# Optimization experiments

Hardware: AMD Instinct MI355X
Metric: run time of the kernel (lower is better)

The kernel has to match this reference:

```python
import jax, jax.numpy as jnp
import numpy as np

L, B, S, KV, H, D, HID, FF = 4, 16, 16, 2048, 6, 128, 768, 2048


def apply_rope(x, positions, max_wavelength=10000.0):
    # x: [B, S, H, D], positions: [B, S]; computed in float32 as in the torch code
    d_half = x.shape[-1] // 2
    freq_exponents = (2.0 / x.shape[-1]) * jnp.arange(d_half, dtype=jnp.float32)
    timescale = max_wavelength ** freq_exponents  # [d_half]
    radians = positions[..., None].astype(jnp.float32) / timescale[None, None, :]
    radians = radians[..., None, :]  # [B, S, 1, d_half]
    sin, cos = jnp.sin(radians), jnp.cos(radians)
    xf = x.astype(jnp.float32)
    x1, x2 = xf[..., :d_half], xf[..., d_half:]
    out = jnp.concatenate([x1 * cos - x2 * sin, x2 * cos + x1 * sin], axis=-1)
    return out.astype(x.dtype)


def rms_norm(x, w, eps=1e-6):
    var = jnp.mean(jnp.square(x.astype(jnp.float32)), axis=-1, keepdims=True)
    return (x.astype(jnp.float32) * jax.lax.rsqrt(var + eps)).astype(x.dtype) * w


def make_att_2d_masks(pad_masks, att_masks):
    # cumsum-comparison prefix-LM / block-causal mask (big_vision style)
    cumsum = jnp.cumsum(att_masks, axis=1)
    att_2d = cumsum[:, None, :] <= cumsum[:, :, None]
    pad_2d = pad_masks[:, None, :] & pad_masks[:, :, None]
    return att_2d & pad_2d


def setup_inputs() -> dict:
    key = jax.random.key(0)
    ks = jax.random.split(key, 20)
    sc = 0.02
    inputs_embeds = jax.random.normal(ks[0], (B, S, HID), jnp.float32)
    position_ids = jnp.broadcast_to(KV + jnp.arange(S, dtype=jnp.int64)[None, :], (B, S))
    pad_masks = jnp.ones((B, KV + S), dtype=bool)
    # prefix-LM: prefix tokens bidirectional (0), expert suffix causal (1)
    att_masks = jnp.concatenate([jnp.zeros((B, KV), jnp.int32), jnp.ones((B, S), jnp.int32)], axis=1)
    k_cache = jax.random.normal(ks[1], (L, B, H, KV, D), jnp.float32)
    v_cache = jax.random.normal(ks[2], (L, B, H, KV, D), jnp.float32)
    p = {
        'Wq': jax.random.normal(ks[3], (L, HID, H * D), jnp.float32) * sc,
        'bq': jnp.zeros((L, H * D), jnp.float32),
        'Wk': jax.random.normal(ks[4], (L, HID, H * D), jnp.float32) * sc,
        'bk': jnp.zeros((L, H * D), jnp.float32),
        'Wv': jax.random.normal(ks[5], (L, HID, H * D), jnp.float32) * sc,
        'bv': jnp.zeros((L, H * D), jnp.float32),
        'Wo': jax.random.normal(ks[6], (L, H * D, HID), jnp.float32) * sc,
        'Wg': jax.random.normal(ks[7], (L, HID, FF), jnp.float32) * sc,
        'Wu': jax.random.normal(ks[8], (L, HID, FF), jnp.float32) * sc,
        'Wd': jax.random.normal(ks[9], (L, FF, HID), jnp.float32) * sc,
        'ln1': jnp.ones((L, HID), jnp.float32),
        'ln2': jnp.ones((L, HID), jnp.float32),
        'norm_f': jnp.ones((HID,), jnp.float32),
    }
    return dict(inputs_embeds=inputs_embeds, position_ids=position_ids, pad_masks=pad_masks,
                att_masks=att_masks, k_cache=k_cache, v_cache=v_cache, **p)


def reference(inputs_embeds, position_ids, pad_masks, att_masks, k_cache, v_cache,
              Wq, bq, Wk, bk, Wv, bv, Wo, Wg, Wu, Wd, ln1, ln2, norm_f):
    b, s, _ = inputs_embeds.shape
    kv = k_cache.shape[3]
    scale = 1.0 / np.sqrt(D)
    # 2D prefix-lm mask over full prefix+suffix; expert queries are the last s rows
    mask2d = make_att_2d_masks(pad_masks, att_masks)[:, kv:, :]  # [B, S, KV+S]
    bias = jnp.where(mask2d[:, None, :, :], 0.0, -1e9).astype(inputs_embeds.dtype)
    h = inputs_embeds
    for l in range(Wq.shape[0]):
        hn = rms_norm(h, ln1[l])
        q = (hn @ Wq[l] + bq[l]).reshape(b, s, H, D)
        k = (hn @ Wk[l] + bk[l]).reshape(b, s, H, D)
        v = (hn @ Wv[l] + bv[l]).reshape(b, s, H, D)
        q = apply_rope(q, position_ids)
        k = apply_rope(k, position_ids)
        qh = jnp.swapaxes(q, 1, 2)  # [B, H, S, D]
        kf = jnp.concatenate([k_cache[l], jnp.swapaxes(k, 1, 2)], axis=2)  # [B, H, KV+S, D]
        vf = jnp.concatenate([v_cache[l], jnp.swapaxes(v, 1, 2)], axis=2)
        scores = jnp.einsum('bhqd,bhkd->bhqk', qh, kf) * scale + bias
        attn = jax.nn.softmax(scores, axis=-1)
        o = jnp.einsum('bhqk,bhkd->bhqd', attn, vf)
        o = jnp.swapaxes(o, 1, 2).reshape(b, s, H * D) @ Wo[l]
        h = h + o
        hn2 = rms_norm(h, ln2[l])
        h = h + (jax.nn.silu(hn2 @ Wg[l]) * (hn2 @ Wu[l])) @ Wd[l]
    return rms_norm(h, norm_f)
```

## Files before the change

### kernel.cpp

```cpp
#include <hip/hip_runtime.h>
#include <hip/hip_bf16.h>

#define LNUM 4
#define BB 16
#define SS 16
#define KVC 2048
#define HH 6
#define DD 128
#define HIDN 768
#define FFN 2048
#define NCH 17
#define ATT_SCALE 0.08838834764831845f
#define VT_PAD 136
#define OSH_PAD 132
#define AP 776
#define AP3 1032

typedef unsigned short u16;
typedef short s16x8 __attribute__((ext_vector_type(8)));
typedef unsigned short u16x4 __attribute__((ext_vector_type(4)));
typedef float f32x4 __attribute__((ext_vector_type(4)));

__device__ __forceinline__ short f2bfs(float f) {
    __hip_bfloat16 h = __float2bfloat16(f);
    return *reinterpret_cast<short*>(&h);
}

__global__ __launch_bounds__(64) void rope_tab_k(float2* __restrict__ tab) {
    int i = blockIdx.x * 64 + threadIdx.x;
    int s = i >> 6, d = i & 63;
    float ts = powf(10000.f, (float)d * (1.f / 64.f));
    float rad = (float)(KVC + s) / ts;
    tab[i] = make_float2(sinf(rad), cosf(rad));
}

__global__ __launch_bounds__(256) void wtrans_all_k(
    const float* __restrict__ Wq, const float* __restrict__ Wk, const float* __restrict__ Wv,
    const float* __restrict__ Wo, const float* __restrict__ Wg, const float* __restrict__ Wu,
    const float* __restrict__ Wd,
    u16* __restrict__ WqT, u16* __restrict__ WkT, u16* __restrict__ WvT, u16* __restrict__ WoT,
    u16* __restrict__ WgT, u16* __restrict__ WuT, u16* __restrict__ WdT) {
    int idx = blockIdx.x, z = blockIdx.y;
    const float* in; u16* out; int K, N, nx, tt;
    if (idx < 432)      { tt = idx % 144; K = 768;  N = 768;  nx = 12;
                          int w = idx / 144;
                          in = (w==0)?Wq:(w==1)?Wk:Wv; out = (w==0)?WqT:(w==1)?WkT:WvT; }
    else if (idx < 576) { tt = idx - 432; K = 768;  N = 768;  nx = 12; in = Wo; out = WoT; }
    else if (idx < 1344){ tt = (idx - 576) % 384; K = 768; N = 2048; nx = 32;
                          in = (idx < 960) ? Wg : Wu; out = (idx < 960) ? WgT : WuT; }
    else                { tt = idx - 1344; K = 2048; N = 768; nx = 12; in = Wd; out = WdT; }
    int n0 = (tt % nx) * 64, k0 = (tt / nx) * 64;
    in  += (size_t)z * K * N;
    out += (size_t)z * K * N;
    __shared__ u16 T[64][65];
    int t = threadIdx.x;
#pragma unroll
    for (int i = 0; i < 16; ++i) {
        int f = i * 256 + t;
        int k = f >> 6, n = f & 63;
        T[k][n] = (u16)f2bfs(in[(size_t)(k0 + k) * N + n0 + n]);
    }
    __syncthreads();
#pragma unroll
    for (int i = 0; i < 2; ++i) {
        int f = i * 256 + t;
        int n = f >> 3, kg = f & 7;
        s16x8 v;
#pragma unroll
        for (int j = 0; j < 8; ++j) v[j] = (short)T[kg * 8 + j][n];
        *(s16x8*)(out + (size_t)(n0 + n) * K + k0 + kg * 8) = v;
    }
}

__global__ __launch_bounds__(64) void rmsnorm_f_k(const float* __restrict__ x,
                                                  const float* __restrict__ w,
                                                  float* __restrict__ y) {
    int row = blockIdx.x, lane = threadIdx.x;
    const float* xp = x + (size_t)row * HIDN + lane * 12;
    float4 a = *(const float4*)xp;
    float4 b = *(const float4*)(xp + 4);
    float4 c = *(const float4*)(xp + 8);
    float s = a.x*a.x + a.y*a.y + a.z*a.z + a.w*a.w
            + b.x*b.x + b.y*b.y + b.z*b.z + b.w*b.w
            + c.x*c.x + c.y*c.y + c.z*c.z + c.w*c.w;
    for (int m = 1; m < 64; m <<= 1) s += __shfl_xor(s, m);
    float rq = rsqrtf(s * (1.f / 768.f) + 1e-6f);
    const float* wp = w + lane * 12;
    float* yp = y + (size_t)row * HIDN + lane * 12;
#pragma unroll
    for (int i = 0; i < 3; ++i) {
        float4 xv = (i == 0) ? a : (i == 1) ? b : c;
        float4 o;
        o.x = xv.x*rq*wp[i*4]; o.y = xv.y*rq*wp[i*4+1];
        o.z = xv.z*rq*wp[i*4+2]; o.w = xv.w*rq*wp[i*4+3];
        *(float4*)(yp + i * 4) = o;
    }
}

__global__ __launch_bounds__(256) void qkv_k(const float* __restrict__ h,
                                             const float* __restrict__ ln1w,
                                             const u16* __restrict__ WqT, const u16* __restrict__ WkT,
                                             const u16* __restrict__ WvT,
                                             const float* __restrict__ bq, const float* __restrict__ bk,
                                             const float* __restrict__ bv,
                                             const float2* __restrict__ tab,
                                             u16* __restrict__ qr, u16* __restrict__ kr,
                                             u16* __restrict__ vr) {
    int x = blockIdx.x, b = blockIdx.y;
    int kind = x / HH, hh = x % HH;
    const u16* Wt = (kind == 0) ? WqT : (kind == 1) ? WkT : WvT;
    const float* bias = (kind == 0) ? bq : (kind == 1) ? bk : bv;
    u16* outp = (kind == 0) ? qr : (kind == 1) ? kr : vr;
    int tid = threadIdx.x, wid = tid >> 6, lane = tid & 63, r = lane & 15, qg = lane >> 4;
    __shared__ u16 A[16][AP];
    float wln[12];
#pragma unroll
    for (int i = 0; i < 12; ++i) wln[i] = ln1w[lane * 12 + i];
#pragma unroll
    for (int i = 0; i < 4; ++i) {
        int row = wid * 4 + i;
        const float* xp = h + (size_t)(b * 16 + row) * HIDN + lane * 12;
        float4 a = *(const float4*)xp;
        float4 bb = *(const float4*)(xp + 4);
        float4 c = *(const float4*)(xp + 8);
        float s = a.x*a.x + a.y*a.y + a.z*a.z + a.w*a.w
                + bb.x*bb.x + bb.y*bb.y + bb.z*bb.z + bb.w*bb.w
                + c.x*c.x + c.y*c.y + c.z*c.z + c.w*c.w;
        for (int m = 1; m < 64; m <<= 1) s += __shfl_xor(s, m);
        float rq = rsqrtf(s * (1.f / 768.f) + 1e-6f);
#pragma unroll
        for (int j = 0; j < 3; ++j) {
            float4 xv = (j == 0) ? a : (j == 1) ? bb : c;
            u16x4 o;
#pragma unroll
            for (int t = 0; t < 4; ++t) o[t] = (u16)f2bfs((&xv.x)[t] * rq * wln[j * 4 + t]);
            *(u16x4*)(&A[row][lane * 12 + j * 4]) = o;
        }
    }
    __syncthreads();
    f32x4 acc0 = (f32x4){0.f,0.f,0.f,0.f};
    f32x4 acc1 = (f32x4){0.f,0.f,0.f,0.f};
    int d1 = wid * 16 + r, d2 = d1 + 64;
#pragma unroll 4
    for (int k0 = 0; k0 < HIDN; k0 += 32) {
        s16x8 a = *(const s16x8*)(&A[r][k0 + qg * 8]);
        s16x8 b0 = *(const s16x8*)(Wt + (size_t)(hh * DD + d1 - r + r) * HIDN + k0 + qg * 8);
        acc0 = __builtin_amdgcn_mfma_f32_16x16x32_bf16(a, b0, acc0, 0, 0, 0);
        s16x8 b1 = *(const s16x8*)(Wt + (size_t)(hh * DD + d2) * HIDN + k0 + qg * 8);
        acc1 = __builtin_amdgcn_mfma_f32_16x16x32_bf16(a, b1, acc1, 0, 0, 0);
    }
    int bh = b * HH + hh;
    float b1v = bias[hh * DD + d1], b2v = bias[hh * DD + d2];
    if (kind < 2) {
#pragma unroll
        for (int v = 0; v < 4; ++v) {
            int s = qg * 4 + v;
            float2 sc = tab[s * 64 + d1];
            float x1 = acc0[v] + b1v;
            float x2 = acc1[v] + b2v;
            outp[(size_t)(bh * 16 + s) * DD + d1] = (u16)f2bfs(x1 * sc.y - x2 * sc.x);
            outp[(size_t)(bh * 16 + s) * DD + d2] = (u16)f2bfs(x2 * sc.y + x1 * sc.x);
        }
    } else {
#pragma unroll
        for (int v = 0; v < 4; ++v) {
            int s = qg * 4 + v;
            outp[(size_t)(bh * 16 + s) * DD + d1] = (u16)f2bfs(acc0[v] + b1v);
            outp[(size_t)(bh * 16 + s) * DD + d2] = (u16)f2bfs(acc1[v] + b2v);
        }
    }
}

__global__ __launch_bounds__(256) void attn_part_k(
    const u16* __restrict__ qr, const u16* __restrict__ kr, const u16* __restrict__ vr,
    const float* __restrict__ kc, const float* __restrict__ vc,
    float* __restrict__ part_o, float* __restrict__ part_ml) {
    int bh = blockIdx.x, ch = blockIdx.y;
    int tid = threadIdx.x, wid = tid >> 6, lane = tid & 63, r = lane & 15, qg = lane >> 4;
    bool isnew = (ch == NCH - 1);
    bool active = !isnew || (wid == 0);
    __shared__ __align__(16) char smem[128 * VT_PAD * 2];
    u16* Vt = (u16*)smem;
    float* Osh = (float*)smem;
    __shared__ __align__(16) u16 Plds[4][512];
    __shared__ float mlsh[4][32];

    const float* vbase_wg = vc + ((size_t)bh * KVC + ch * 128) * DD;
    const u16* vrn = vr + (size_t)bh * SS * DD;

    if (!isnew) {
#pragma unroll
        for (int i = 0; i < 8; ++i) {
            int flat = i * 256 + tid;
            int c4 = flat & 31, rp = flat >> 5;
            const float* p0 = vbase_wg + (size_t)(2 * rp) * DD + c4 * 4;
            float4 a = *(const float4*)p0;
            float4 b = *(const float4*)(p0 + DD);
#pragma unroll
            for (int c = 0; c < 4; ++c) {
                unsigned lo = (unsigned)(u16)f2bfs((&a.x)[c]);
                unsigned hi = (unsigned)(u16)f2bfs((&b.x)[c]);
                *(unsigned*)(Vt + (size_t)(c4 * 4 + c) * VT_PAD + 2 * rp) = lo | (hi << 16);
            }
        }
    } else {
#pragma unroll
        for (int i = 0; i < 16; ++i) {
            int flat = i * 256 + tid;
            int key = flat >> 7, d = flat & 127;
            u16 v = (key < SS) ? vrn[(size_t)key * DD + d] : (u16)0;
            Vt[(size_t)d * VT_PAD + key] = v;
        }
    }
    __syncthreads();

    float mrow[4] = {-1e30f, -1e30f, -1e30f, -1e30f};
    float lrow[4] = {0.f, 0.f, 0.f, 0.f};
    f32x4 oacc[8];
#pragma unroll
    for (int nt = 0; nt < 8; ++nt) oacc[nt] = (f32x4){0.f, 0.f, 0.f, 0.f};

    if (active) {
        s16x8 aq[4];
#pragma unroll
        for (int kk = 0; kk < 4; ++kk)
            aq[kk] = *(const s16x8*)(qr + (size_t)(bh * 16 + r) * DD + kk * 32 + qg * 8);
        const float* kbase = kc + ((size_t)bh * KVC + ch * 128 + wid * 32) * DD;
        const u16* krn = kr + (size_t)bh * SS * DD;

        f32x4 st[2];
        st[0] = (f32x4){0.f,0.f,0.f,0.f};
        st[1] = (f32x4){0.f,0.f,0.f,0.f};
#pragma unroll
        for (int t = 0; t < 2; ++t) {
            if (isnew && t == 1) continue;
#pragma unroll
            for (int kk = 0; kk < 4; ++kk) {
                s16x8 bk;
                if (isnew) {
                    bk = *(const s16x8*)(krn + (size_t)(t * 16 + r) * DD + kk * 32 + qg * 8);
                } else {
                    const float* p = kbase + (size_t)(t * 16 + r) * DD + kk * 32 + qg * 8;
                    float4 xx = *(const float4*)p;
                    float4 yy = *(const float4*)(p + 4);
                    bk[0]=f2bfs(xx.x); bk[1]=f2bfs(xx.y); bk[2]=f2bfs(xx.z); bk[3]=f2bfs(xx.w);
                    bk[4]=f2bfs(yy.x); bk[5]=f2bfs(yy.y); bk[6]=f2bfs(yy.z); bk[7]=f2bfs(yy.w);
                }
                st[t] = __builtin_amdgcn_mfma_f32_16x16x32_bf16(aq[kk], bk, st[t], 0, 0, 0);
            }
        }
#pragma unroll
        for (int t = 0; t < 2; ++t)
#pragma unroll
            for (int v = 0; v < 4; ++v) st[t][v] *= ATT_SCALE;
        if (isnew) {
#pragma unroll
            for (int v = 0; v < 4; ++v) {
                if (r > qg * 4 + v) st[0][v] = -1e9f;
                st[1][v] = -1e9f;
            }
        }
#pragma unroll
        for (int v = 0; v < 4; ++v) {
            float xm = fmaxf(st[0][v], st[1][v]);
            for (int msk = 1; msk < 16; msk <<= 1) xm = fmaxf(xm, __shfl_xor(xm, msk));
            mrow[v] = xm;
        }
#pragma unroll
        for (int t = 0; t < 2; ++t)
#pragma unroll
            for (int v = 0; v < 4; ++v) st[t][v] = __expf(st[t][v] - mrow[v]);
#pragma unroll
        for (int v = 0; v < 4; ++v) {
            float ss = st[0][v] + st[1][v];
            for (int msk = 1; msk < 16; msk <<= 1) ss += __shfl_xor(ss, msk);
            lrow[v] = ss;
        }
#pragma unroll
        for (int t = 0; t < 2; ++t)
#pragma unroll
            for (int v = 0; v < 4; ++v)
                Plds[wid][(qg * 4 + v) * 32 + t * 16 + r] = (u16)f2bfs(st[t][v]);
        s16x8 ap = *(const s16x8*)(&Plds[wid][r * 32 + qg * 8]);
#pragma unroll
        for (int nt = 0; nt < 8; ++nt) {
            s16x8 bv = *(const s16x8*)(Vt + (size_t)(nt * 16 + r) * VT_PAD + wid * 32 + qg * 8);
            oacc[nt] = __builtin_amdgcn_mfma_f32_16x16x32_bf16(ap, bv, oacc[nt], 0, 0, 0);
        }
    }
    __syncthreads();
#pragma unroll
    for (int nt = 0; nt < 8; ++nt)
#pragma unroll
        for (int v = 0; v < 4; ++v)
            Osh[(size_t)(wid * 16 + qg * 4 + v) * OSH_PAD + nt * 16 + r] = oacc[nt][v];
    if (r == 0) {
#pragma unroll
        for (int v = 0; v < 4; ++v) {
            mlsh[wid][qg * 4 + v] = mrow[v];
            mlsh[wid][16 + qg * 4 + v] = lrow[v];
        }
    }
    __syncthreads();
    int q = tid >> 4, dg = tid & 15;
    float M = -1e30f;
#pragma unroll
    for (int w = 0; w < 4; ++w) M = fmaxf(M, mlsh[w][q]);
    float L = 0.f, wgt[4];
#pragma unroll
    for (int w = 0; w < 4; ++w) {
        wgt[w] = __expf(mlsh[w][q] - M);
        L += mlsh[w][16 + q] * wgt[w];
    }
    float o[8];
#pragma unroll
    for (int j = 0; j < 8; ++j) o[j] = 0.f;
#pragma unroll
    for (int w = 0; w < 4; ++w) {
        const float* op = Osh + (size_t)(w * 16 + q) * OSH_PAD + dg * 8;
        float4 a = *(const float4*)op;
        float4 b = *(const float4*)(op + 4);
        o[0]+=wgt[w]*a.x; o[1]+=wgt[w]*a.y; o[2]+=wgt[w]*a.z; o[3]+=wgt[w]*a.w;
        o[4]+=wgt[w]*b.x; o[5]+=wgt[w]*b.y; o[6]+=wgt[w]*b.z; o[7]+=wgt[w]*b.w;
    }
    float* po = part_o + ((size_t)bh * NCH + ch) * (SS * DD) + q * DD + dg * 8;
    float4 o0; o0.x=o[0]; o0.y=o[1]; o0.z=o[2]; o0.w=o[3];
    float4 o1; o1.x=o[4]; o1.y=o[5]; o1.z=o[6]; o1.w=o[7];
    *(float4*)po = o0;
    *(float4*)(po + 4) = o1;
    if (dg == 0) {
        float* pm = part_ml + ((size_t)bh * NCH + ch) * 32;
        pm[q] = M;
        pm[16 + q] = L;
    }
}

__global__ __launch_bounds__(256) void attn_comb_k(const float* __restrict__ part_o,
                                                   const float* __restrict__ part_ml,
                                                   u16* __restrict__ oa) {
    int bh = blockIdx.x, tid = threadIdx.x;
    __shared__ float sw[NCH][16], sLi[16];
    if (tid < 16) {
        float M = -1e30f;
        for (int c = 0; c < NCH; ++c) M = fmaxf(M, part_ml[((size_t)bh * NCH + c) * 32 + tid]);
        float L = 0.f;
        for (int c = 0; c < NCH; ++c) {
            const float* pm = part_ml + ((size_t)bh * NCH + c) * 32;
            float w = __expf(pm[tid] - M);
            sw[c][tid] = w;
            L += pm[16 + tid] * w;
        }
        sLi[tid] = 1.f / L;
    }
    __syncthreads();
    int q = tid >> 4, dg = tid & 15;
    float o[8];
#pragma unroll
    for (int j = 0; j < 8; ++j) o[j] = 0.f;
    for (int c = 0; c < NCH; ++c) {
        const float* po = part_o + ((size_t)bh * NCH + c) * (SS * DD) + q * DD + dg * 8;
        float4 a = *(const float4*)po;
        float4 b = *(const float4*)(po + 4);
        float w = sw[c][q];
        o[0]+=w*a.x; o[1]+=w*a.y; o[2]+=w*a.z; o[3]+=w*a.w;
        o[4]+=w*b.x; o[5]+=w*b.y; o[6]+=w*b.z; o[7]+=w*b.w;
    }
    float inv = sLi[q];
    int b = bh / HH, h = bh % HH;
    u16* yp = oa + (size_t)(b * SS + q) * HIDN + h * DD + dg * 8;
    s16x8 ov;
#pragma unroll
    for (int j = 0; j < 8; ++j) ov[j] = f2bfs(o[j] * inv);
    *(s16x8*)yp = ov;
}

__global__ __launch_bounds__(256) void wo_res_k(const u16* __restrict__ oa,
                                                const u16* __restrict__ WoT,
                                                float* __restrict__ h) {
    int tid = threadIdx.x, wid = tid >> 6, lane = tid & 63, r = lane & 15, qg = lane >> 4;
    int b = blockIdx.y;
    __shared__ u16 A[16][AP];
#pragma unroll
    for (int i = 0; i < 6; ++i) {
        int idx8 = i * 256 + tid;
        int row = idx8 / 96, c8 = idx8 % 96;
        *(s16x8*)(&A[row][c8 * 8]) =
            *(const s16x8*)(oa + (size_t)(b * 16 + row) * HIDN + c8 * 8);
    }
    __syncthreads();
    int n0 = blockIdx.x * 64 + wid * 16;
    f32x4 acc = (f32x4){0.f, 0.f, 0.f, 0.f};
#pragma unroll 4
    for (int k0 = 0; k0 < HIDN; k0 += 32) {
        s16x8 a  = *(const s16x8*)(&A[r][k0 + qg * 8]);
        s16x8 bw = *(const s16x8*)(WoT + (size_t)(n0 + r) * HIDN + k0 + qg * 8);
        acc = __builtin_amdgcn_mfma_f32_16x16x32_bf16(a, bw, acc, 0, 0, 0);
    }
#pragma unroll
    for (int v = 0; v < 4; ++v)
        h[(size_t)(b * 16 + qg * 4 + v) * HIDN + n0 + r] += acc[v];
}

__global__ __launch_bounds__(256) void ln2gu_k(const float* __restrict__ h,
                                               const float* __restrict__ ln2w,
                                               const u16* __restrict__ WgT,
                                               const u16* __restrict__ WuT,
                                               u16* __restrict__ F) {
    int tid = threadIdx.x, wid = tid >> 6, lane = tid & 63, r = lane & 15, qg = lane >> 4;
    int m0 = blockIdx.y * 16;
    __shared__ u16 A[16][AP];
    float wln[12];
#pragma unroll
    for (int i = 0; i < 12; ++i) wln[i] = ln2w[lane * 12 + i];
#pragma unroll
    for (int i = 0; i < 4; ++i) {
        int row = wid * 4 + i;
        const float* xp = h + (size_t)(m0 + row) * HIDN + lane * 12;
        float4 a = *(const float4*)xp;
        float4 bb = *(const float4*)(xp + 4);
        float4 c = *(const float4*)(xp + 8);
        float s = a.x*a.x + a.y*a.y + a.z*a.z + a.w*a.w
                + bb.x*bb.x + bb.y*bb.y + bb.z*bb.z + bb.w*bb.w
                + c.x*c.x + c.y*c.y + c.z*c.z + c.w*c.w;
        for (int m = 1; m < 64; m <<= 1) s += __shfl_xor(s, m);
        float rq = rsqrtf(s * (1.f / 768.f) + 1e-6f);
#pragma unroll
        for (int j = 0; j < 3; ++j) {
            float4 xv = (j == 0) ? a : (j == 1) ? bb : c;
            u16x4 o;
#pragma unroll
            for (int t = 0; t < 4; ++t) o[t] = (u16)f2bfs((&xv.x)[t] * rq * wln[j * 4 + t]);
            *(u16x4*)(&A[row][lane * 12 + j * 4]) = o;
        }
    }
    __syncthreads();
    int n0 = blockIdx.x * 64 + wid * 16;
    f32x4 ag = (f32x4){0.f, 0.f, 0.f, 0.f};
    f32x4 au = (f32x4){0.f, 0.f, 0.f, 0.f};
#pragma unroll 4
    for (int k0 = 0; k0 < HIDN; k0 += 32) {
        s16x8 a  = *(const s16x8*)(&A[r][k0 + qg * 8]);
        s16x8 bg = *(const s16x8*)(WgT + (size_t)(n0 + r) * HIDN + k0 + qg * 8);
        ag = __builtin_amdgcn_mfma_f32_16x16x32_bf16(a, bg, ag, 0, 0, 0);
        s16x8 bu = *(const s16x8*)(WuT + (size_t)(n0 + r) * HIDN + k0 + qg * 8);
        au = __builtin_amdgcn_mfma_f32_16x16x32_bf16(a, bu, au, 0, 0, 0);
    }
#pragma unroll
    for (int v = 0; v < 4; ++v) {
        float gv = ag[v], uv = au[v];
        float f = gv / (1.f + __expf(-gv)) * uv;
        F[(size_t)(m0 + qg * 4 + v) * FFN + n0 + r] = (u16)f2bfs(f);
    }
}

__global__ __launch_bounds__(256) void down_res_k(const u16* __restrict__ F,
                                                  const u16* __restrict__ WdT,
                                                  float* __restrict__ H) {
    int tid = threadIdx.x, wid = tid >> 6, lane = tid & 63, r = lane & 15, qg = lane >> 4;
    int m0 = blockIdx.y * 16;
    int kbeg = blockIdx.z * 1024;
    __shared__ u16 A[16][AP3];
#pragma unroll
    for (int i = 0; i < 8; ++i) {
        int idx8 = i * 256 + tid;
        int row = idx8 >> 7, c8 = idx8 & 127;
        *(s16x8*)(&A[row][c8 * 8]) =
            *(const s16x8*)(F + (size_t)(m0 + row) * FFN + kbeg + c8 * 8);
    }
    __syncthreads();
    int n0 = blockIdx.x * 64 + wid * 16;
    f32x4 acc = (f32x4){0.f, 0.f, 0.f, 0.f};
#pragma unroll 4
    for (int k0 = 0; k0 < 1024; k0 += 32) {
        s16x8 a  = *(const s16x8*)(&A[r][k0 + qg * 8]);
        s16x8 bw = *(const s16x8*)(WdT + (size_t)(n0 + r) * FFN + kbeg + k0 + qg * 8);
        acc = __builtin_amdgcn_mfma_f32_16x16x32_bf16(a, bw, acc, 0, 0, 0);
    }
#pragma unroll
    for (int v = 0; v < 4; ++v)
        atomicAdd(&H[(size_t)(m0 + qg * 4 + v) * HIDN + n0 + r], acc[v]);
}

extern "C" void kernel_launch(void* const* d_in, const int* in_sizes, int n_in,
                              void* d_out, int out_size, void* d_ws, size_t ws_size,
                              hipStream_t stream) {
    (void)in_sizes; (void)n_in; (void)out_size; (void)ws_size;
    const float* emb     = (const float*)d_in[0];
    const float* k_cache = (const float*)d_in[4];
    const float* v_cache = (const float*)d_in[5];
    const float* Wq = (const float*)d_in[6];
    const float* bq = (const float*)d_in[7];
    const float* Wk = (const float*)d_in[8];
    const float* bk = (const float*)d_in[9];
    const float* Wv = (const float*)d_in[10];
    const float* bv = (const float*)d_in[11];
    const float* Wo = (const float*)d_in[12];
    const float* Wg = (const float*)d_in[13];
    const float* Wu = (const float*)d_in[14];
    const float* Wd = (const float*)d_in[15];
    const float* ln1 = (const float*)d_in[16];
    const float* ln2 = (const float*)d_in[17];
    const float* normf = (const float*)d_in[18];
    float* out = (float*)d_out;

    char* p = (char*)d_ws;
    auto alloc = [&](size_t bytes) { void* r = p; p += (bytes + 255) & ~255ull; return r; };
    const size_t WQKV = (size_t)HIDN * HH * DD;
    const size_t WMLP = (size_t)HIDN * FFN;
    u16* WqT = (u16*)alloc(LNUM * WQKV * 2);
    u16* WkT = (u16*)alloc(LNUM * WQKV * 2);
    u16* WvT = (u16*)alloc(LNUM * WQKV * 2);
    u16* WoT = (u16*)alloc(LNUM * WQKV * 2);
    u16* WgT = (u16*)alloc(LNUM * WMLP * 2);
    u16* WuT = (u16*)alloc(LNUM * WMLP * 2);
    u16* WdT = (u16*)alloc(LNUM * WMLP * 2);
    const int TOK = BB * SS;
    const size_t EMB_N = (size_t)TOK * HIDN;
    float* h  = (float*)alloc(EMB_N * 4);
    u16* qr   = (u16*)alloc((size_t)BB * HH * SS * DD * 2);
    u16* kr   = (u16*)alloc((size_t)BB * HH * SS * DD * 2);
    u16* vr   = (u16*)alloc((size_t)BB * HH * SS * DD * 2);
    u16* oa   = (u16*)alloc(EMB_N * 2);
    u16* fb   = (u16*)alloc((size_t)TOK * FFN * 2);
    float* po  = (float*)alloc((size_t)96 * NCH * SS * DD * 4);
    float* pml = (float*)alloc((size_t)96 * NCH * 32 * 4);
    float2* tab = (float2*)alloc(16 * 64 * sizeof(float2));

    rope_tab_k<<<16, 64, 0, stream>>>(tab);
    wtrans_all_k<<<dim3(1728, LNUM), 256, 0, stream>>>(Wq, Wk, Wv, Wo, Wg, Wu, Wd,
                                                       WqT, WkT, WvT, WoT, WgT, WuT, WdT);
    hipMemcpyAsync(h, emb, EMB_N * sizeof(float), hipMemcpyDeviceToDevice, stream);

    const size_t KVOFF = (size_t)BB * HH * KVC * DD;
    for (int l = 0; l < LNUM; ++l) {
        qkv_k<<<dim3(3 * HH, BB), 256, 0, stream>>>(h, ln1 + l * HIDN,
            WqT + l * WQKV, WkT + l * WQKV, WvT + l * WQKV,
            bq + l * HH * DD, bk + l * HH * DD, bv + l * HH * DD, tab, qr, kr, vr);
        attn_part_k<<<dim3(BB * HH, NCH), 256, 0, stream>>>(qr, kr, vr,
            k_cache + (size_t)l * KVOFF, v_cache + (size_t)l * KVOFF, po, pml);
        attn_comb_k<<<BB * HH, 256, 0, stream>>>(po, pml, oa);
        wo_res_k<<<dim3(12, BB), 256, 0, stream>>>(oa, WoT + l * WQKV, h);
        ln2gu_k<<<dim3(32, BB), 256, 0, stream>>>(h, ln2 + l * HIDN,
            WgT + l * WMLP, WuT + l * WMLP, fb);
        down_res_k<<<dim3(12, BB, 2), 256, 0, stream>>>(fb, WdT + l * WMLP, h);
    }
    rmsnorm_f_k<<<TOK, 64, 0, stream>>>(h, normf, out);
}
```

Before: 438.7 us.

## Fuse all per-layer kernels into one persistent cooperative megakernel with grid syncs

Replaces the roughly 26 separate kernel launches (weight transpose, rope table, QKV, attention partial and combine, Wo, gate/up, down, final norm) with one cooperative persistent kernel. The blocks loop over the former grids' work items and use grid-wide syncs between stages. The aim is to remove launch overhead and inter-kernel gaps in a latency-bound workload of small GEMMs. In exchange, each stage adds a grid barrier, occupancy is capped by a shared 39KB LDS buffer and the launch bounds, and some stages have far fewer work items than resident blocks.

```diff
diff --git a/kernel.cpp b/kernel.cpp
--- a/kernel.cpp
+++ b/kernel.cpp
@@ -1,5 +1,8 @@
 #include <hip/hip_runtime.h>
 #include <hip/hip_bf16.h>
+#include <hip/hip_cooperative_groups.h>
+
+namespace cg = cooperative_groups;
 
 #define LNUM 4
 #define BB 16
@@ -26,523 +29,555 @@
     return *reinterpret_cast<short*>(&h);
 }
 
-__global__ __launch_bounds__(64) void rope_tab_k(float2* __restrict__ tab) {
-    int i = blockIdx.x * 64 + threadIdx.x;
-    int s = i >> 6, d = i & 63;
-    float ts = powf(10000.f, (float)d * (1.f / 64.f));
-    float rad = (float)(KVC + s) / ts;
-    tab[i] = make_float2(sinf(rad), cosf(rad));
-}
-
-__global__ __launch_bounds__(256) void wtrans_all_k(
-    const float* __restrict__ Wq, const float* __restrict__ Wk, const float* __restrict__ Wv,
-    const float* __restrict__ Wo, const float* __restrict__ Wg, const float* __restrict__ Wu,
-    const float* __restrict__ Wd,
-    u16* __restrict__ WqT, u16* __restrict__ WkT, u16* __restrict__ WvT, u16* __restrict__ WoT,
-    u16* __restrict__ WgT, u16* __restrict__ WuT, u16* __restrict__ WdT) {
-    int idx = blockIdx.x, z = blockIdx.y;
-    const float* in; u16* out; int K, N, nx, tt;
-    if (idx < 432)      { tt = idx % 144; K = 768;  N = 768;  nx = 12;
-                          int w = idx / 144;
-                          in = (w==0)?Wq:(w==1)?Wk:Wv; out = (w==0)?WqT:(w==1)?WkT:WvT; }
-    else if (idx < 576) { tt = idx - 432; K = 768;  N = 768;  nx = 12; in = Wo; out = WoT; }
-    else if (idx < 1344){ tt = (idx - 576) % 384; K = 768; N = 2048; nx = 32;
-                          in = (idx < 960) ? Wg : Wu; out = (idx < 960) ? WgT : WuT; }
-    else                { tt = idx - 1344; K = 2048; N = 768; nx = 12; in = Wd; out = WdT; }
-    int n0 = (tt % nx) * 64, k0 = (tt / nx) * 64;
-    in  += (size_t)z * K * N;
-    out += (size_t)z * K * N;
-    __shared__ u16 T[64][65];
-    int t = threadIdx.x;
-#pragma unroll
-    for (int i = 0; i < 16; ++i) {
-        int f = i * 256 + t;
-        int k = f >> 6, n = f & 63;
-        T[k][n] = (u16)f2bfs(in[(size_t)(k0 + k) * N + n0 + n]);
+struct MegaArgs {
+    const float *emb, *kc, *vc;
+    const float *Wq, *Wk, *Wv, *Wo, *Wg, *Wu, *Wd;
+    const float *bq, *bk, *bv, *ln1, *ln2, *normf;
+    u16 *WqT, *WkT, *WvT, *WoT, *WgT, *WuT, *WdT;
+    float *h;
+    u16 *qr, *kr, *vr, *oa, *fb;
+    float *po, *pml;
+    float2 *tab;
+    float *out;
+};
+
+__global__ __launch_bounds__(256, 3) void mega_k(MegaArgs a) {
+    cg::grid_group gg = cg::this_grid();
+    __shared__ __align__(16) char SM[39424];
+    const int tid = threadIdx.x, wid = tid >> 6, lane = tid & 63;
+    const int r = lane & 15, qg = lane >> 4;
+    const size_t WQKV = (size_t)HIDN * HH * DD;
+    const size_t WMLP = (size_t)HIDN * FFN;
+    const size_t KVOFF = (size_t)BB * HH * KVC * DD;
+
+    {
+        u16 (*T)[65] = (u16(*)[65])SM;
+        for (int t = blockIdx.x; t < 6912 + 192 + 1; t += gridDim.x) {
+            if (t < 6912) {
+                int z = t / 1728, idx = t % 1728;
+                const float* in; u16* out; int K, N, nx, tt;
+                if (idx < 432)      { tt = idx % 144; K = 768;  N = 768;  nx = 12;
+                                      int w = idx / 144;
+                                      in = (w==0)?a.Wq:(w==1)?a.Wk:a.Wv;
+                                      out = (w==0)?a.WqT:(w==1)?a.WkT:a.WvT; }
+                else if (idx < 576) { tt = idx - 432; K = 768;  N = 768;  nx = 12;
+                                      in = a.Wo; out = a.WoT; }
+                else if (idx < 1344){ tt = (idx - 576) % 384; K = 768; N = 2048; nx = 32;
+                                      in = (idx < 960) ? a.Wg : a.Wu;
+                                      out = (idx < 960) ? a.WgT : a.WuT; }
+                else                { tt = idx - 1344; K = 2048; N = 768; nx = 12;
+                                      in = a.Wd; out = a.WdT; }
+                int n0 = (tt % nx) * 64, k0 = (tt / nx) * 64;
+                in  += (size_t)z * K * N;
+                out += (size_t)z * K * N;
+#pragma unroll
+                for (int i = 0; i < 16; ++i) {
+                    int f = i * 256 + tid;
+                    int k = f >> 6, n = f & 63;
+                    T[k][n] = (u16)f2bfs(in[(size_t)(k0 + k) * N + n0 + n]);
+                }
+                __syncthreads();
+#pragma unroll
+                for (int i = 0; i < 2; ++i) {
+                    int f = i * 256 + tid;
+                    int n = f >> 3, kg = f & 7;
+                    s16x8 v;
+#pragma unroll
+                    for (int j = 0; j < 8; ++j) v[j] = (short)T[kg * 8 + j][n];
+                    *(s16x8*)(out + (size_t)(n0 + n) * K + k0 + kg * 8) = v;
+                }
+            } else if (t < 6912 + 192) {
+                int c = t - 6912;
+                int base = c * 256 + tid;
+                ((float4*)a.h)[base] = ((const float4*)a.emb)[base];
+            } else {
+#pragma unroll
+                for (int j = 0; j < 4; ++j) {
+                    int id = tid * 4 + j;
+                    int s = id >> 6, d = id & 63;
+                    float ts = powf(10000.f, (float)d * (1.f / 64.f));
+                    float rad = (float)(KVC + s) / ts;
+                    a.tab[id] = make_float2(sinf(rad), cosf(rad));
+                }
+            }
+            __syncthreads();
+        }
     }
-    __syncthreads();
-#pragma unroll
-    for (int i = 0; i < 2; ++i) {
-        int f = i * 256 + t;
-        int n = f >> 3, kg = f & 7;
-        s16x8 v;
-#pragma unroll
-        for (int j = 0; j < 8; ++j) v[j] = (short)T[kg * 8 + j][n];
-        *(s16x8*)(out + (size_t)(n0 + n) * K + k0 + kg * 8) = v;
+    gg.sync();
+
+    for (int l = 0; l < LNUM; ++l) {
+        const u16* WqTl = a.WqT + l * WQKV;
+        const u16* WkTl = a.WkT + l * WQKV;
+        const u16* WvTl = a.WvT + l * WQKV;
+        const u16* WoTl = a.WoT + l * WQKV;
+        const u16* WgTl = a.WgT + l * WMLP;
+        const u16* WuTl = a.WuT + l * WMLP;
+        const u16* WdTl = a.WdT + l * WMLP;
+        const float* ln1w = a.ln1 + l * HIDN;
+        const float* ln2w = a.ln2 + l * HIDN;
+        const float* kc = a.kc + (size_t)l * KVOFF;
+        const float* vc = a.vc + (size_t)l * KVOFF;
+
+        {
+            u16 (*A)[AP] = (u16(*)[AP])SM;
+            for (int t = blockIdx.x; t < 3 * HH * BB; t += gridDim.x) {
+                int x = t % (3 * HH), b = t / (3 * HH);
+                int kind = x / HH, hh = x % HH;
+                const u16* Wt = (kind == 0) ? WqTl : (kind == 1) ? WkTl : WvTl;
+                const float* bias = ((kind == 0) ? a.bq : (kind == 1) ? a.bk : a.bv) + l * HH * DD;
+                u16* outp = (kind == 0) ? a.qr : (kind == 1) ? a.kr : a.vr;
+                float wln[12];
+#pragma unroll
+                for (int i = 0; i < 12; ++i) wln[i] = ln1w[lane * 12 + i];
+#pragma unroll
+                for (int i = 0; i < 4; ++i) {
+                    int row = wid * 4 + i;
+                    const float* xp = a.h + (size_t)(b * 16 + row) * HIDN + lane * 12;
+                    float4 av = *(const float4*)xp;
+                    float4 bv = *(const float4*)(xp + 4);
+                    float4 cv = *(const float4*)(xp + 8);
+                    float s = av.x*av.x + av.y*av.y + av.z*av.z + av.w*av.w
+                            + bv.x*bv.x + bv.y*bv.y + bv.z*bv.z + bv.w*bv.w
+                            + cv.x*cv.x + cv.y*cv.y + cv.z*cv.z + cv.w*cv.w;
+                    for (int m = 1; m < 64; m <<= 1) s += __shfl_xor(s, m);
+                    float rq = rsqrtf(s * (1.f / 768.f) + 1e-6f);
+#pragma unroll
+                    for (int j = 0; j < 3; ++j) {
+                        float4 xv = (j == 0) ? av : (j == 1) ? bv : cv;
+                        u16x4 o;
+#pragma unroll
+                        for (int u = 0; u < 4; ++u) o[u] = (u16)f2bfs((&xv.x)[u] * rq * wln[j * 4 + u]);
+                        *(u16x4*)(&A[row][lane * 12 + j * 4]) = o;
+                    }
+                }
+                __syncthreads();
+                f32x4 acc0 = (f32x4){0.f,0.f,0.f,0.f};
+                f32x4 acc1 = (f32x4){0.f,0.f,0.f,0.f};
+                int d1 = wid * 16 + r, d2 = d1 + 64;
+#pragma unroll 4
+                for (int k0 = 0; k0 < HIDN; k0 += 32) {
+                    s16x8 av = *(const s16x8*)(&A[r][k0 + qg * 8]);
+                    s16x8 b0 = *(const s16x8*)(Wt + (size_t)(hh * DD + d1) * HIDN + k0 + qg * 8);
+                    acc0 = __builtin_amdgcn_mfma_f32_16x16x32_bf16(av, b0, acc0, 0, 0, 0);
+                    s16x8 b1 = *(const s16x8*)(Wt + (size_t)(hh * DD + d2) * HIDN + k0 + qg * 8);
+                    acc1 = __builtin_amdgcn_mfma_f32_16x16x32_bf16(av, b1, acc1, 0, 0, 0);
+                }
+                int bh = b * HH + hh;
+                float b1v = bias[hh * DD + d1], b2v = bias[hh * DD + d2];
+                if (kind < 2) {
+#pragma unroll
+                    for (int v = 0; v < 4; ++v) {
+                        int s = qg * 4 + v;
+                        float2 sc = a.tab[s * 64 + d1];
+                        float x1 = acc0[v] + b1v;
+                        float x2 = acc1[v] + b2v;
+                        outp[(size_t)(bh * 16 + s) * DD + d1] = (u16)f2bfs(x1 * sc.y - x2 * sc.x);
+                        outp[(size_t)(bh * 16 + s) * DD + d2] = (u16)f2bfs(x2 * sc.y + x1 * sc.x);
+                    }
+                } else {
+#pragma unroll
+                    for (int v = 0; v < 4; ++v) {
+                        int s = qg * 4 + v;
+                        outp[(size_t)(bh * 16 + s) * DD + d1] = (u16)f2bfs(acc0[v] + b1v);
+                        outp[(size_t)(bh * 16 + s) * DD + d2] = (u16)f2bfs(acc1[v] + b2v);
+                    }
+                }
+                __syncthreads();
+            }
+        }
+        gg.sync();
+
+        {
+            u16* Vt = (u16*)SM;
+            float* Osh = (float*)SM;
+            u16 (*Plds)[512] = (u16(*)[512])(SM + 34816);
+            float (*mlsh)[32] = (float(*)[32])(SM + 34816 + 4096);
+            for (int t = blockIdx.x; t < 96 * NCH; t += gridDim.x) {
+                int bh = t % 96, ch = t / 96;
+                bool isnew = (ch == NCH - 1);
+                bool active = !isnew || (wid == 0);
+                const float* vbase_wg = vc + ((size_t)bh * KVC + ch * 128) * DD;
+                const u16* vrn = a.vr + (size_t)bh * SS * DD;
+
+                if (!isnew) {
+#pragma unroll
+                    for (int i = 0; i < 8; ++i) {
+                        int flat = i * 256 + tid;
+                        int c4 = flat & 31, rp = flat >> 5;
+                        const float* p0 = vbase_wg + (size_t)(2 * rp) * DD + c4 * 4;
+                        float4 av = *(const float4*)p0;
+                        float4 bv = *(const float4*)(p0 + DD);
+#pragma unroll
+                        for (int c = 0; c < 4; ++c) {
+                            unsigned lo = (unsigned)(u16)f2bfs((&av.x)[c]);
+                            unsigned hi = (unsigned)(u16)f2bfs((&bv.x)[c]);
+                            *(unsigned*)(Vt + (size_t)(c4 * 4 + c) * VT_PAD + 2 * rp) = lo | (hi << 16);
+                        }
+                    }
+                } else {
+#pragma unroll
+                    for (int i = 0; i < 16; ++i) {
+                        int flat = i * 256 + tid;
+                        int key = flat >> 7, d = flat & 127;
+                        u16 v = (key < SS) ? vrn[(size_t)key * DD + d] : (u16)0;
+                        Vt[(size_t)d * VT_PAD + key] = v;
+                    }
+                }
+                __syncthreads();
+
+                float mrow[4] = {-1e30f, -1e30f, -1e30f, -1e30f};
+                float lrow[4] = {0.f, 0.f, 0.f, 0.f};
+                f32x4 oacc[8];
+#pragma unroll
+                for (int nt = 0; nt < 8; ++nt) oacc[nt] = (f32x4){0.f, 0.f, 0.f, 0.f};
+
+                if (active) {
+                    s16x8 aq[4];
+#pragma unroll
+                    for (int kk = 0; kk < 4; ++kk)
+                        aq[kk] = *(const s16x8*)(a.qr + (size_t)(bh * 16 + r) * DD + kk * 32 + qg * 8);
+                    const float* kbase = kc + ((size_t)bh * KVC + ch * 128 + wid * 32) * DD;
+                    const u16* krn = a.kr + (size_t)bh * SS * DD;
+
+                    f32x4 st[2];
+                    st[0] = (f32x4){0.f,0.f,0.f,0.f};
+                    st[1] = (f32x4){0.f,0.f,0.f,0.f};
+#pragma unroll
+                    for (int tt = 0; tt < 2; ++tt) {
+                        if (isnew && tt == 1) continue;
+#pragma unroll
+                        for (int kk = 0; kk < 4; ++kk) {
+                            s16x8 bk;
+                            if (isnew) {
+                                bk = *(const s16x8*)(krn + (size_t)(tt * 16 + r) * DD + kk * 32 + qg * 8);
+                            } else {
+                                const float* p = kbase + (size_t)(tt * 16 + r) * DD + kk * 32 + qg * 8;
+                                float4 xx = *(const float4*)p;
+                                float4 yy = *(const float4*)(p + 4);
+                                bk[0]=f2bfs(xx.x); bk[1]=f2bfs(xx.y); bk[2]=f2bfs(xx.z); bk[3]=f2bfs(xx.w);
+                                bk[4]=f2bfs(yy.x); bk[5]=f2bfs(yy.y); bk[6]=f2bfs(yy.z); bk[7]=f2bfs(yy.w);
+                            }
+                            st[tt] = __builtin_amdgcn_mfma_f32_16x16x32_bf16(aq[kk], bk, st[tt], 0, 0, 0);
+                        }
+                    }
+#pragma unroll
+                    for (int tt = 0; tt < 2; ++tt)
+#pragma unroll
+                        for (int v = 0; v < 4; ++v) st[tt][v] *= ATT_SCALE;
+                    if (isnew) {
+#pragma unroll
+                        for (int v = 0; v < 4; ++v) {
+                            if (r > qg * 4 + v) st[0][v] = -1e9f;
+                            st[1][v] = -1e9f;
+                        }
+                    }
+#pragma unroll
+                    for (int v = 0; v < 4; ++v) {
+                        float xm = fmaxf(st[0][v], st[1][v]);
+                        for (int msk = 1; msk < 16; msk <<= 1) xm = fmaxf(xm, __shfl_xor(xm, msk));
+                        mrow[v] = xm;
+                    }
+#pragma unroll
+                    for (int tt = 0; tt < 2; ++tt)
+#pragma unroll
+                        for (int v = 0; v < 4; ++v) st[tt][v] = __expf(st[tt][v] - mrow[v]);
+#pragma unroll
+                    for (int v = 0; v < 4; ++v) {
+                        float ss = st[0][v] + st[1][v];
+                        for (int msk = 1; msk < 16; msk <<= 1) ss += __shfl_xor(ss, msk);
+                        lrow[v] = ss;
+                    }
+#pragma unroll
+                    for (int tt = 0; tt < 2; ++tt)
+#pragma unroll
+                        for (int v = 0; v < 4; ++v)
+                            Plds[wid][(qg * 4 + v) * 32 + tt * 16 + r] = (u16)f2bfs(st[tt][v]);
+                    s16x8 ap = *(const s16x8*)(&Plds[wid][r * 32 + qg * 8]);
+#pragma unroll
+                    for (int nt = 0; nt < 8; ++nt) {
+                        s16x8 bv = *(const s16x8*)(Vt + (size_t)(nt * 16 + r) * VT_PAD + wid * 32 + qg * 8);
+                        oacc[nt] = __builtin_amdgcn_mfma_f32_16x16x32_bf16(ap, bv, oacc[nt], 0, 0, 0);
+                    }
+                }
+                __syncthreads();
+#pragma unroll
+                for (int nt = 0; nt < 8; ++nt)
+#pragma unroll
+                    for (int v = 0; v < 4; ++v)
+                        Osh[(size_t)(wid * 16 + qg * 4 + v) * OSH_PAD + nt * 16 + r] = oacc[nt][v];
+                if (r == 0) {
+#pragma unroll
+                    for (int v = 0; v < 4; ++v) {
+                        mlsh[wid][qg * 4 + v] = mrow[v];
+                        mlsh[wid][16 + qg * 4 + v] = lrow[v];
+                    }
+                }
+                __syncthreads();
+                int q = tid >> 4, dg = tid & 15;
+                float M = -1e30f;
+#pragma unroll
+                for (int w = 0; w < 4; ++w) M = fmaxf(M, mlsh[w][q]);
+                float L = 0.f, wgt[4];
+#pragma unroll
+                for (int w = 0; w < 4; ++w) {
+                    wgt[w] = __expf(mlsh[w][q] - M);
+                    L += mlsh[w][16 + q] * wgt[w];
+                }
+                float o[8];
+#pragma unroll
+                for (int j = 0; j < 8; ++j) o[j] = 0.f;
+#pragma unroll
+                for (int w = 0; w < 4; ++w) {
+                    const float* op = Osh + (size_t)(w * 16 + q) * OSH_PAD + dg * 8;
+                    float4 av = *(const float4*)op;
+                    float4 bv = *(const float4*)(op + 4);
+                    o[0]+=wgt[w]*av.x; o[1]+=wgt[w]*av.y; o[2]+=wgt[w]*av.z; o[3]+=wgt[w]*av.w;
+                    o[4]+=wgt[w]*bv.x; o[5]+=wgt[w]*bv.y; o[6]+=wgt[w]*bv.z; o[7]+=wgt[w]*bv.w;
+                }
+                float* po = a.po + ((size_t)bh * NCH + ch) * (SS * DD) + q * DD + dg * 8;
+                float4 o0; o0.x=o[0]; o0.y=o[1]; o0.z=o[2]; o0.w=o[3];
+                float4 o1; o1.x=o[4]; o1.y=o[5]; o1.z=o[6]; o1.w=o[7];
+                *(float4*)po = o0;
+                *(float4*)(po + 4) = o1;
+                if (dg == 0) {
+                    float* pm = a.pml + ((size_t)bh * NCH + ch) * 32;
+                    pm[q] = M;
+                    pm[16 + q] = L;
+                }
+                __syncthreads();
+            }
+        }
+        gg.sync();
+
+        {
+            float (*sw)[16] = (float(*)[16])SM;
+            float* sLi = (float*)(SM + NCH * 16 * 4);
+            for (int t = blockIdx.x; t < 96; t += gridDim.x) {
+                int bh = t;
+                if (tid < 16) {
+                    float M = -1e30f;
+                    for (int c = 0; c < NCH; ++c)
+                        M = fmaxf(M, a.pml[((size_t)bh * NCH + c) * 32 + tid]);
+                    float L = 0.f;
+                    for (int c = 0; c < NCH; ++c) {
+                        const float* pm = a.pml + ((size_t)bh * NCH + c) * 32;
+                        float w = __expf(pm[tid] - M);
+                        sw[c][tid] = w;
+                        L += pm[16 + tid] * w;
+                    }
+                    sLi[tid] = 1.f / L;
+                }
+                __syncthreads();
+                int q = tid >> 4, dg = tid & 15;
+                float o[8];
+#pragma unroll
+                for (int j = 0; j < 8; ++j) o[j] = 0.f;
+                for (int c = 0; c < NCH; ++c) {
+                    const float* po = a.po + ((size_t)bh * NCH + c) * (SS * DD) + q * DD + dg * 8;
+                    float4 av = *(const float4*)po;
+                    float4 bv = *(const float4*)(po + 4);
+                    float w = sw[c][q];
+                    o[0]+=w*av.x; o[1]+=w*av.y; o[2]+=w*av.z; o[3]+=w*av.w;
+                    o[4]+=w*bv.x; o[5]+=w*bv.y; o[6]+=w*bv.z; o[7]+=w*bv.w;
+                }
+                float inv = sLi[q];
+                int b = bh / HH, hh = bh % HH;
+                u16* yp = a.oa + (size_t)(b * SS + q) * HIDN + hh * DD + dg * 8;
+                s16x8 ov;
+#pragma unroll
+                for (int j = 0; j < 8; ++j) ov[j] = f2bfs(o[j] * inv);
+                *(s16x8*)yp = ov;
+                __syncthreads();
+            }
+        }
+        gg.sync();
+
+        {
+            u16 (*A)[AP] = (u16(*)[AP])SM;
+            for (int t = blockIdx.x; t < 12 * BB; t += gridDim.x) {
+                int nx = t % 12, b = t / 12;
+#pragma unroll
+                for (int i = 0; i < 6; ++i) {
+                    int idx8 = i * 256 + tid;
+                    int row = idx8 / 96, c8 = idx8 % 96;
+                    *(s16x8*)(&A[row][c8 * 8]) =
+                        *(const s16x8*)(a.oa + (size_t)(b * 16 + row) * HIDN + c8 * 8);
+                }
+                __syncthreads();
+                int n0 = nx * 64 + wid * 16;
+                f32x4 acc = (f32x4){0.f, 0.f, 0.f, 0.f};
+#pragma unroll 4
+                for (int k0 = 0; k0 < HIDN; k0 += 32) {
+                    s16x8 av = *(const s16x8*)(&A[r][k0 + qg * 8]);
+                    s16x8 bw = *(const s16x8*)(WoTl + (size_t)(n0 + r) * HIDN + k0 + qg * 8);
+                    acc = __builtin_amdgcn_mfma_f32_16x16x32_bf16(av, bw, acc, 0, 0, 0);
+                }
+#pragma unroll
+                for (int v = 0; v < 4; ++v)
+                    a.h[(size_t)(b * 16 + qg * 4 + v) * HIDN + n0 + r] += acc[v];
+                __syncthreads();
+            }
+        }
+        gg.sync();
+
+        {
+            u16 (*A)[AP] = (u16(*)[AP])SM;
+            for (int t = blockIdx.x; t < 32 * BB; t += gridDim.x) {
+                int nx = t % 32, mb = t / 32;
+                int m0 = mb * 16;
+                float wln[12];
+#pragma unroll
+                for (int i = 0; i < 12; ++i) wln[i] = ln2w[lane * 12 + i];
+#pragma unroll
+                for (int i = 0; i < 4; ++i) {
+                    int row = wid * 4 + i;
+                    const float* xp = a.h + (size_t)(m0 + row) * HIDN + lane * 12;
+                    float4 av = *(const float4*)xp;
+                    float4 bv = *(const float4*)(xp + 4);
+                    float4 cv = *(const float4*)(xp + 8);
+                    float s = av.x*av.x + av.y*av.y + av.z*av.z + av.w*av.w
+                            + bv.x*bv.x + bv.y*bv.y + bv.z*bv.z + bv.w*bv.w
+                            + cv.x*cv.x + cv.y*cv.y + cv.z*cv.z + cv.w*cv.w;
+                    for (int m = 1; m < 64; m <<= 1) s += __shfl_xor(s, m);
+                    float rq = rsqrtf(s * (1.f / 768.f) + 1e-6f);
+#pragma unroll
+                    for (int j = 0; j < 3; ++j) {
+                        float4 xv = (j == 0) ? av : (j == 1) ? bv : cv;
+                        u16x4 o;
+#pragma unroll
+                        for (int u = 0; u < 4; ++u) o[u] = (u16)f2bfs((&xv.x)[u] * rq * wln[j * 4 + u]);
+                        *(u16x4*)(&A[row][lane * 12 + j * 4]) = o;
+                    }
+                }
+                __syncthreads();
+                int n0 = nx * 64 + wid * 16;
+                f32x4 ag = (f32x4){0.f, 0.f, 0.f, 0.f};
+                f32x4 au = (f32x4){0.f, 0.f, 0.f, 0.f};
+#pragma unroll 4
+                for (int k0 = 0; k0 < HIDN; k0 += 32) {
+                    s16x8 av = *(const s16x8*)(&A[r][k0 + qg * 8]);
+                    s16x8 bg = *(const s16x8*)(WgTl + (size_t)(n0 + r) * HIDN + k0 + qg * 8);
+                    ag = __builtin_amdgcn_mfma_f32_16x16x32_bf16(av, bg, ag, 0, 0, 0);
+                    s16x8 bu = *(const s16x8*)(WuTl + (size_t)(n0 + r) * HIDN + k0 + qg * 8);
+                    au = __builtin_amdgcn_mfma_f32_16x16x32_bf16(av, bu, au, 0, 0, 0);
+                }
+#pragma unroll
+                for (int v = 0; v < 4; ++v) {
+                    float gv = ag[v], uv = au[v];
+                    float f = gv / (1.f + __expf(-gv)) * uv;
+                    a.fb[(size_t)(m0 + qg * 4 + v) * FFN + n0 + r] = (u16)f2bfs(f);
+                }
+                __syncthreads();
+            }
+        }
+        gg.sync();
+
+        {
+            u16 (*A)[AP3] = (u16(*)[AP3])SM;
+            for (int t = blockIdx.x; t < 12 * BB * 2; t += gridDim.x) {
+                int nx = t % 12, mb = (t / 12) % BB, ks = t / (12 * BB);
+                int m0 = mb * 16;
+                int kbeg = ks * 1024;
+#pragma unroll
+                for (int i = 0; i < 8; ++i) {
+                    int idx8 = i * 256 + tid;
+                    int row = idx8 >> 7, c8 = idx8 & 127;
+                    *(s16x8*)(&A[row][c8 * 8]) =
+                        *(const s16x8*)(a.fb + (size_t)(m0 + row) * FFN + kbeg + c8 * 8);
+                }
+                __syncthreads();
+                int n0 = nx * 64 + wid * 16;
+                f32x4 acc = (f32x4){0.f, 0.f, 0.f, 0.f};
+#pragma unroll 4
+                for (int k0 = 0; k0 < 1024; k0 += 32) {
+                    s16x8 av = *(const s16x8*)(&A[r][k0 + qg * 8]);
+                    s16x8 bw = *(const s16x8*)(WdTl + (size_t)(n0 + r) * FFN + kbeg + k0 + qg * 8);
+                    acc = __builtin_amdgcn_mfma_f32_16x16x32_bf16(av, bw, acc, 0, 0, 0);
+                }
+#pragma unroll
+                for (int v = 0; v < 4; ++v)
+                    atomicAdd(&a.h[(size_t)(m0 + qg * 4 + v) * HIDN + n0 + r], acc[v]);
+                __syncthreads();
+            }
+        }
+        gg.sync();
     }
-}
-
-__global__ __launch_bounds__(64) void rmsnorm_f_k(const float* __restrict__ x,
-                                                  const float* __restrict__ w,
-                                                  float* __restrict__ y) {
-    int row = blockIdx.x, lane = threadIdx.x;
-    const float* xp = x + (size_t)row * HIDN + lane * 12;
-    float4 a = *(const float4*)xp;
-    float4 b = *(const float4*)(xp + 4);
-    float4 c = *(const float4*)(xp + 8);
-    float s = a.x*a.x + a.y*a.y + a.z*a.z + a.w*a.w
-            + b.x*b.x + b.y*b.y + b.z*b.z + b.w*b.w
-            + c.x*c.x + c.y*c.y + c.z*c.z + c.w*c.w;
-    for (int m = 1; m < 64; m <<= 1) s += __shfl_xor(s, m);
-    float rq = rsqrtf(s * (1.f / 768.f) + 1e-6f);
-    const float* wp = w + lane * 12;
-    float* yp = y + (size_t)row * HIDN + lane * 12;
-#pragma unroll
-    for (int i = 0; i < 3; ++i) {
-        float4 xv = (i == 0) ? a : (i == 1) ? b : c;
-        float4 o;
-        o.x = xv.x*rq*wp[i*4]; o.y = xv.y*rq*wp[i*4+1];
-        o.z = xv.z*rq*wp[i*4+2]; o.w = xv.w*rq*wp[i*4+3];
-        *(float4*)(yp + i * 4) = o;
-    }
-}
-
-__global__ __launch_bounds__(256) void qkv_k(const float* __restrict__ h,
-                                             const float* __restrict__ ln1w,
-                                             const u16* __restrict__ WqT, const u16* __restrict__ WkT,
-                                             const u16* __restrict__ WvT,
-                                             const float* __restrict__ bq, const float* __restrict__ bk,
-                                             const float* __restrict__ bv,
-                                             const float2* __restrict__ tab,
-                                             u16* __restrict__ qr, u16* __restrict__ kr,
-                                             u16* __restrict__ vr) {
-    int x = blockIdx.x, b = blockIdx.y;
-    int kind = x / HH, hh = x % HH;
-    const u16* Wt = (kind == 0) ? WqT : (kind == 1) ? WkT : WvT;
-    const float* bias = (kind == 0) ? bq : (kind == 1) ? bk : bv;
-    u16* outp = (kind == 0) ? qr : (kind == 1) ? kr : vr;
-    int tid = threadIdx.x, wid = tid >> 6, lane = tid & 63, r = lane & 15, qg = lane >> 4;
-    __shared__ u16 A[16][AP];
-    float wln[12];
-#pragma unroll
-    for (int i = 0; i < 12; ++i) wln[i] = ln1w[lane * 12 + i];
-#pragma unroll
-    for (int i = 0; i < 4; ++i) {
-        int row = wid * 4 + i;
-        const float* xp = h + (size_t)(b * 16 + row) * HIDN + lane * 12;
-        float4 a = *(const float4*)xp;
-        float4 bb = *(const float4*)(xp + 4);
-        float4 c = *(const float4*)(xp + 8);
-        float s = a.x*a.x + a.y*a.y + a.z*a.z + a.w*a.w
-                + bb.x*bb.x + bb.y*bb.y + bb.z*bb.z + bb.w*bb.w
-                + c.x*c.x + c.y*c.y + c.z*c.z + c.w*c.w;
+
+    for (int t = blockIdx.x; t < 64; t += gridDim.x) {
+        int row = t * 4 + wid;
+        const float* xp = a.h + (size_t)row * HIDN + lane * 12;
+        float4 av = *(const float4*)xp;
+        float4 bv = *(const float4*)(xp + 4);
+        float4 cv = *(const float4*)(xp + 8);
+        float s = av.x*av.x + av.y*av.y + av.z*av.z + av.w*av.w
+                + bv.x*bv.x + bv.y*bv.y + bv.z*bv.z + bv.w*bv.w
+                + cv.x*cv.x + cv.y*cv.y + cv.z*cv.z + cv.w*cv.w;
         for (int m = 1; m < 64; m <<= 1) s += __shfl_xor(s, m);
         float rq = rsqrtf(s * (1.f / 768.f) + 1e-6f);
-#pragma unroll
-        for (int j = 0; j < 3; ++j) {
-            float4 xv = (j == 0) ? a : (j == 1) ? bb : c;
-            u16x4 o;
-#pragma unroll
-            for (int t = 0; t < 4; ++t) o[t] = (u16)f2bfs((&xv.x)[t] * rq * wln[j * 4 + t]);
-            *(u16x4*)(&A[row][lane * 12 + j * 4]) = o;
+        const float* wp = a.normf + lane * 12;
+        float* yp = a.out + (size_t)row * HIDN + lane * 12;
+#pragma unroll
+        for (int i = 0; i < 3; ++i) {
+            float4 xv = (i == 0) ? av : (i == 1) ? bv : cv;
+            float4 o;
+            o.x = xv.x*rq*wp[i*4];   o.y = xv.y*rq*wp[i*4+1];
+            o.z = xv.z*rq*wp[i*4+2]; o.w = xv.w*rq*wp[i*4+3];
+            *(float4*)(yp + i * 4) = o;
         }
     }
-    __syncthreads();
-    f32x4 acc0 = (f32x4){0.f,0.f,0.f,0.f};
-    f32x4 acc1 = (f32x4){0.f,0.f,0.f,0.f};
-    int d1 = wid * 16 + r, d2 = d1 + 64;
-#pragma unroll 4
-    for (int k0 = 0; k0 < HIDN; k0 += 32) {
-        s16x8 a = *(const s16x8*)(&A[r][k0 + qg * 8]);
-        s16x8 b0 = *(const s16x8*)(Wt + (size_t)(hh * DD + d1 - r + r) * HIDN + k0 + qg * 8);
-        acc0 = __builtin_amdgcn_mfma_f32_16x16x32_bf16(a, b0, acc0, 0, 0, 0);
-        s16x8 b1 = *(const s16x8*)(Wt + (size_t)(hh * DD + d2) * HIDN + k0 + qg * 8);
-        acc1 = __builtin_amdgcn_mfma_f32_16x16x32_bf16(a, b1, acc1, 0, 0, 0);
-    }
-    int bh = b * HH + hh;
-    float b1v = bias[hh * DD + d1], b2v = bias[hh * DD + d2];
-    if (kind < 2) {
-#pragma unroll
-        for (int v = 0; v < 4; ++v) {
-            int s = qg * 4 + v;
-            float2 sc = tab[s * 64 + d1];
-            float x1 = acc0[v] + b1v;
-            float x2 = acc1[v] + b2v;
-            outp[(size_t)(bh * 16 + s) * DD + d1] = (u16)f2bfs(x1 * sc.y - x2 * sc.x);
-            outp[(size_t)(bh * 16 + s) * DD + d2] = (u16)f2bfs(x2 * sc.y + x1 * sc.x);
-        }
-    } else {
-#pragma unroll
-        for (int v = 0; v < 4; ++v) {
-            int s = qg * 4 + v;
-            outp[(size_t)(bh * 16 + s) * DD + d1] = (u16)f2bfs(acc0[v] + b1v);
-            outp[(size_t)(bh * 16 + s) * DD + d2] = (u16)f2bfs(acc1[v] + b2v);
-        }
-    }
-}
-
-__global__ __launch_bounds__(256) void attn_part_k(
-    const u16* __restrict__ qr, const u16* __restrict__ kr, const u16* __restrict__ vr,
-    const float* __restrict__ kc, const float* __restrict__ vc,
-    float* __restrict__ part_o, float* __restrict__ part_ml) {
-    int bh = blockIdx.x, ch = blockIdx.y;
-    int tid = threadIdx.x, wid = tid >> 6, lane = tid & 63, r = lane & 15, qg = lane >> 4;
-    bool isnew = (ch == NCH - 1);
-    bool active = !isnew || (wid == 0);
-    __shared__ __align__(16) char smem[128 * VT_PAD * 2];
-    u16* Vt = (u16*)smem;
-    float* Osh = (float*)smem;
-    __shared__ __align__(16) u16 Plds[4][512];
-    __shared__ float mlsh[4][32];
-
-    const float* vbase_wg = vc + ((size_t)bh * KVC + ch * 128) * DD;
-    const u16* vrn = vr + (size_t)bh * SS * DD;
-
-    if (!isnew) {
-#pragma unroll
-        for (int i = 0; i < 8; ++i) {
-            int flat = i * 256 + tid;
-            int c4 = flat & 31, rp = flat >> 5;
-            const float* p0 = vbase_wg + (size_t)(2 * rp) * DD + c4 * 4;
-            float4 a = *(const float4*)p0;
-            float4 b = *(const float4*)(p0 + DD);
-#pragma unroll
-            for (int c = 0; c < 4; ++c) {
-                unsigned lo = (unsigned)(u16)f2bfs((&a.x)[c]);
-                unsigned hi = (unsigned)(u16)f2bfs((&b.x)[c]);
-                *(unsigned*)(Vt + (size_t)(c4 * 4 + c) * VT_PAD + 2 * rp) = lo | (hi << 16);
-            }
-        }
-    } else {
-#pragma unroll
-        for (int i = 0; i < 16; ++i) {
-            int flat = i * 256 + tid;
-            int key = flat >> 7, d = flat & 127;
-            u16 v = (key < SS) ? vrn[(size_t)key * DD + d] : (u16)0;
-            Vt[(size_t)d * VT_PAD + key] = v;
-        }
-    }
-    __syncthreads();
-
-    float mrow[4] = {-1e30f, -1e30f, -1e30f, -1e30f};
-    float lrow[4] = {0.f, 0.f, 0.f, 0.f};
-    f32x4 oacc[8];
-#pragma unroll
-    for (int nt = 0; nt < 8; ++nt) oacc[nt] = (f32x4){0.f, 0.f, 0.f, 0.f};
-
-    if (active) {
-        s16x8 aq[4];
-#pragma unroll
-        for (int kk = 0; kk < 4; ++kk)
-            aq[kk] = *(const s16x8*)(qr + (size_t)(bh * 16 + r) * DD + kk * 32 + qg * 8);
-        const float* kbase = kc + ((size_t)bh * KVC + ch * 128 + wid * 32) * DD;
-        const u16* krn = kr + (size_t)bh * SS * DD;
-
-        f32x4 st[2];
-        st[0] = (f32x4){0.f,0.f,0.f,0.f};
-        st[1] = (f32x4){0.f,0.f,0.f,0.f};
-#pragma unroll
-        for (int t = 0; t < 2; ++t) {
-            if (isnew && t == 1) continue;
-#pragma unroll
-            for (int kk = 0; kk < 4; ++kk) {
-                s16x8 bk;
-                if (isnew) {
-                    bk = *(const s16x8*)(krn + (size_t)(t * 16 + r) * DD + kk * 32 + qg * 8);
-                } else {
-                    const float* p = kbase + (size_t)(t * 16 + r) * DD + kk * 32 + qg * 8;
-                    float4 xx = *(const float4*)p;
-                    float4 yy = *(const float4*)(p + 4);
-                    bk[0]=f2bfs(xx.x); bk[1]=f2bfs(xx.y); bk[2]=f2bfs(xx.z); bk[3]=f2bfs(xx.w);
-                    bk[4]=f2bfs(yy.x); bk[5]=f2bfs(yy.y); bk[6]=f2bfs(yy.z); bk[7]=f2bfs(yy.w);
-                }
-                st[t] = __builtin_amdgcn_mfma_f32_16x16x32_bf16(aq[kk], bk, st[t], 0, 0, 0);
-            }
-        }
-#pragma unroll
-        for (int t = 0; t < 2; ++t)
-#pragma unroll
-            for (int v = 0; v < 4; ++v) st[t][v] *= ATT_SCALE;
-        if (isnew) {
-#pragma unroll
-            for (int v = 0; v < 4; ++v) {
-                if (r > qg * 4 + v) st[0][v] = -1e9f;
-                st[1][v] = -1e9f;
-            }
-        }
-#pragma unroll
-        for (int v = 0; v < 4; ++v) {
-            float xm = fmaxf(st[0][v], st[1][v]);
-            for (int msk = 1; msk < 16; msk <<= 1) xm = fmaxf(xm, __shfl_xor(xm, msk));
-            mrow[v] = xm;
-        }
-#pragma unroll
-        for (int t = 0; t < 2; ++t)
-#pragma unroll
-            for (int v = 0; v < 4; ++v) st[t][v] = __expf(st[t][v] - mrow[v]);
-#pragma unroll
-        for (int v = 0; v < 4; ++v) {
-            float ss = st[0][v] + st[1][v];
-            for (int msk = 1; msk < 16; msk <<= 1) ss += __shfl_xor(ss, msk);
-            lrow[v] = ss;
-        }
-#pragma unroll
-        for (int t = 0; t < 2; ++t)
-#pragma unroll
-            for (int v = 0; v < 4; ++v)
-                Plds[wid][(qg * 4 + v) * 32 + t * 16 + r] = (u16)f2bfs(st[t][v]);
-        s16x8 ap = *(const s16x8*)(&Plds[wid][r * 32 + qg * 8]);
-#pragma unroll
-        for (int nt = 0; nt < 8; ++nt) {
-            s16x8 bv = *(const s16x8*)(Vt + (size_t)(nt * 16 + r) * VT_PAD + wid * 32 + qg * 8);
-            oacc[nt] = __builtin_amdgcn_mfma_f32_16x16x32_bf16(ap, bv, oacc[nt], 0, 0, 0);
-        }
-    }
-    __syncthreads();
-#pragma unroll
-    for (int nt = 0; nt < 8; ++nt)
-#pragma unroll
-        for (int v = 0; v < 4; ++v)
-            Osh[(size_t)(wid * 16 + qg * 4 + v) * OSH_PAD + nt * 16 + r] = oacc[nt][v];
-    if (r == 0) {
-#pragma unroll
-        for (int v = 0; v < 4; ++v) {
-            mlsh[wid][qg * 4 + v] = mrow[v];
-            mlsh[wid][16 + qg * 4 + v] = lrow[v];
-        }
-    }
-    __syncthreads();
-    int q = tid >> 4, dg = tid & 15;
-    float M = -1e30f;
-#pragma unroll
-    for (int w = 0; w < 4; ++w) M = fmaxf(M, mlsh[w][q]);
-    float L = 0.f, wgt[4];
-#pragma unroll
-    for (int w = 0; w < 4; ++w) {
-        wgt[w] = __expf(mlsh[w][q] - M);
-        L += mlsh[w][16 + q] * wgt[w];
-    }
-    float o[8];
-#pragma unroll
-    for (int j = 0; j < 8; ++j) o[j] = 0.f;
-#pragma unroll
-    for (int w = 0; w < 4; ++w) {
-        const float* op = Osh + (size_t)(w * 16 + q) * OSH_PAD + dg * 8;
-        float4 a = *(const float4*)op;
-        float4 b = *(const float4*)(op + 4);
-        o[0]+=wgt[w]*a.x; o[1]+=wgt[w]*a.y; o[2]+=wgt[w]*a.z; o[3]+=wgt[w]*a.w;
-        o[4]+=wgt[w]*b.x; o[5]+=wgt[w]*b.y; o[6]+=wgt[w]*b.z; o[7]+=wgt[w]*b.w;
-    }
-    float* po = part_o + ((size_t)bh * NCH + ch) * (SS * DD) + q * DD + dg * 8;
-    float4 o0; o0.x=o[0]; o0.y=o[1]; o0.z=o[2]; o0.w=o[3];
-    float4 o1; o1.x=o[4]; o1.y=o[5]; o1.z=o[6]; o1.w=o[7];
-    *(float4*)po = o0;
-    *(float4*)(po + 4) = o1;
-    if (dg == 0) {
-        float* pm = part_ml + ((size_t)bh * NCH + ch) * 32;
-        pm[q] = M;
-        pm[16 + q] = L;
-    }
-}
-
-__global__ __launch_bounds__(256) void attn_comb_k(const float* __restrict__ part_o,
-                                                   const float* __restrict__ part_ml,
-                                                   u16* __restrict__ oa) {
-    int bh = blockIdx.x, tid = threadIdx.x;
-    __shared__ float sw[NCH][16], sLi[16];
-    if (tid < 16) {
-        float M = -1e30f;
-        for (int c = 0; c < NCH; ++c) M = fmaxf(M, part_ml[((size_t)bh * NCH + c) * 32 + tid]);
-        float L = 0.f;
-        for (int c = 0; c < NCH; ++c) {
-            const float* pm = part_ml + ((size_t)bh * NCH + c) * 32;
-            float w = __expf(pm[tid] - M);
-            sw[c][tid] = w;
-            L += pm[16 + tid] * w;
-        }
-        sLi[tid] = 1.f / L;
-    }
-    __syncthreads();
-    int q = tid >> 4, dg = tid & 15;
-    float o[8];
-#pragma unroll
-    for (int j = 0; j < 8; ++j) o[j] = 0.f;
-    for (int c = 0; c < NCH; ++c) {
-        const float* po = part_o + ((size_t)bh * NCH + c) * (SS * DD) + q * DD + dg * 8;
-        float4 a = *(const float4*)po;
-        float4 b = *(const float4*)(po + 4);
-        float w = sw[c][q];
-        o[0]+=w*a.x; o[1]+=w*a.y; o[2]+=w*a.z; o[3]+=w*a.w;
-        o[4]+=w*b.x; o[5]+=w*b.y; o[6]+=w*b.z; o[7]+=w*b.w;
-    }
-    float inv = sLi[q];
-    int b = bh / HH, h = bh % HH;
-    u16* yp = oa + (size_t)(b * SS + q) * HIDN + h * DD + dg * 8;
-    s16x8 ov;
-#pragma unroll
-    for (int j = 0; j < 8; ++j) ov[j] = f2bfs(o[j] * inv);
-    *(s16x8*)yp = ov;
-}
-
-__global__ __launch_bounds__(256) void wo_res_k(const u16* __restrict__ oa,
-                                                const u16* __restrict__ WoT,
-                                                float* __restrict__ h) {
-    int tid = threadIdx.x, wid = tid >> 6, lane = tid & 63, r = lane & 15, qg = lane >> 4;
-    int b = blockIdx.y;
-    __shared__ u16 A[16][AP];
-#pragma unroll
-    for (int i = 0; i < 6; ++i) {
-        int idx8 = i * 256 + tid;
-        int row = idx8 / 96, c8 = idx8 % 96;
-        *(s16x8*)(&A[row][c8 * 8]) =
-            *(const s16x8*)(oa + (size_t)(b * 16 + row) * HIDN + c8 * 8);
-    }
-    __syncthreads();
-    int n0 = blockIdx.x * 64 + wid * 16;
-    f32x4 acc = (f32x4){0.f, 0.f, 0.f, 0.f};
-#pragma unroll 4
-    for (int k0 = 0; k0 < HIDN; k0 += 32) {
-        s16x8 a  = *(const s16x8*)(&A[r][k0 + qg * 8]);
-        s16x8 bw = *(const s16x8*)(WoT + (size_t)(n0 + r) * HIDN + k0 + qg * 8);
-        acc = __builtin_amdgcn_mfma_f32_16x16x32_bf16(a, bw, acc, 0, 0, 0);
-    }
-#pragma unroll
-    for (int v = 0; v < 4; ++v)
-        h[(size_t)(b * 16 + qg * 4 + v) * HIDN + n0 + r] += acc[v];
-}
-
-__global__ __launch_bounds__(256) void ln2gu_k(const float* __restrict__ h,
-                                               const float* __restrict__ ln2w,
-                                               const u16* __restrict__ WgT,
-                                               const u16* __restrict__ WuT,
-                                               u16* __restrict__ F) {
-    int tid = threadIdx.x, wid = tid >> 6, lane = tid & 63, r = lane & 15, qg = lane >> 4;
-    int m0 = blockIdx.y * 16;
-    __shared__ u16 A[16][AP];
-    float wln[12];
-#pragma unroll
-    for (int i = 0; i < 12; ++i) wln[i] = ln2w[lane * 12 + i];
-#pragma unroll
-    for (int i = 0; i < 4; ++i) {
-        int row = wid * 4 + i;
-        const float* xp = h + (size_t)(m0 + row) * HIDN + lane * 12;
-        float4 a = *(const float4*)xp;
-        float4 bb = *(const float4*)(xp + 4);
-        float4 c = *(const float4*)(xp + 8);
-        float s = a.x*a.x + a.y*a.y + a.z*a.z + a.w*a.w
-                + bb.x*bb.x + bb.y*bb.y + bb.z*bb.z + bb.w*bb.w
-                + c.x*c.x + c.y*c.y + c.z*c.z + c.w*c.w;
-        for (int m = 1; m < 64; m <<= 1) s += __shfl_xor(s, m);
-        float rq = rsqrtf(s * (1.f / 768.f) + 1e-6f);
-#pragma unroll
-        for (int j = 0; j < 3; ++j) {
-            float4 xv = (j == 0) ? a : (j == 1) ? bb : c;
-            u16x4 o;
-#pragma unroll
-            for (int t = 0; t < 4; ++t) o[t] = (u16)f2bfs((&xv.x)[t] * rq * wln[j * 4 + t]);
-            *(u16x4*)(&A[row][lane * 12 + j * 4]) = o;
-        }
-    }
-    __syncthreads();
-    int n0 = blockIdx.x * 64 + wid * 16;
-    f32x4 ag = (f32x4){0.f, 0.f, 0.f, 0.f};
-    f32x4 au = (f32x4){0.f, 0.f, 0.f, 0.f};
-#pragma unroll 4
-    for (int k0 = 0; k0 < HIDN; k0 += 32) {
-        s16x8 a  = *(const s16x8*)(&A[r][k0 + qg * 8]);
-        s16x8 bg = *(const s16x8*)(WgT + (size_t)(n0 + r) * HIDN + k0 + qg * 8);
-        ag = __builtin_amdgcn_mfma_f32_16x16x32_bf16(a, bg, ag, 0, 0, 0);
-        s16x8 bu = *(const s16x8*)(WuT + (size_t)(n0 + r) * HIDN + k0 + qg * 8);
-        au = __builtin_amdgcn_mfma_f32_16x16x32_bf16(a, bu, au, 0, 0, 0);
-    }
-#pragma unroll
-    for (int v = 0; v < 4; ++v) {
-        float gv = ag[v], uv = au[v];
-        float f = gv / (1.f + __expf(-gv)) * uv;
-        F[(size_t)(m0 + qg * 4 + v) * FFN + n0 + r] = (u16)f2bfs(f);
-    }
-}
-
-__global__ __launch_bounds__(256) void down_res_k(const u16* __restrict__ F,
-                                                  const u16* __restrict__ WdT,
-                                                  float* __restrict__ H) {
-    int tid = threadIdx.x, wid = tid >> 6, lane = tid & 63, r = lane & 15, qg = lane >> 4;
-    int m0 = blockIdx.y * 16;
-    int kbeg = blockIdx.z * 1024;
-    __shared__ u16 A[16][AP3];
-#pragma unroll
-    for (int i = 0; i < 8; ++i) {
-        int idx8 = i * 256 + tid;
-        int row = idx8 >> 7, c8 = idx8 & 127;
-        *(s16x8*)(&A[row][c8 * 8]) =
-            *(const s16x8*)(F + (size_t)(m0 + row) * FFN + kbeg + c8 * 8);
-    }
-    __syncthreads();
-    int n0 = blockIdx.x * 64 + wid * 16;
-    f32x4 acc = (f32x4){0.f, 0.f, 0.f, 0.f};
-#pragma unroll 4
-    for (int k0 = 0; k0 < 1024; k0 += 32) {
-        s16x8 a  = *(const s16x8*)(&A[r][k0 + qg * 8]);
-        s16x8 bw = *(const s16x8*)(WdT + (size_t)(n0 + r) * FFN + kbeg + k0 + qg * 8);
-        acc = __builtin_amdgcn_mfma_f32_16x16x32_bf16(a, bw, acc, 0, 0, 0);
-    }
-#pragma unroll
-    for (int v = 0; v < 4; ++v)
-        atomicAdd(&H[(size_t)(m0 + qg * 4 + v) * HIDN + n0 + r], acc[v]);
 }
 
 extern "C" void kernel_launch(void* const* d_in, const int* in_sizes, int n_in,
                               void* d_out, int out_size, void* d_ws, size_t ws_size,
                               hipStream_t stream) {
     (void)in_sizes; (void)n_in; (void)out_size; (void)ws_size;
-    const float* emb     = (const float*)d_in[0];
-    const float* k_cache = (const float*)d_in[4];
-    const float* v_cache = (const float*)d_in[5];
-    const float* Wq = (const float*)d_in[6];
-    const float* bq = (const float*)d_in[7];
-    const float* Wk = (const float*)d_in[8];
-    const float* bk = (const float*)d_in[9];
-    const float* Wv = (const float*)d_in[10];
-    const float* bv = (const float*)d_in[11];
-    const float* Wo = (const float*)d_in[12];
-    const float* Wg = (const float*)d_in[13];
-    const float* Wu = (const float*)d_in[14];
-    const float* Wd = (const float*)d_in[15];
-    const float* ln1 = (const float*)d_in[16];
-    const float* ln2 = (const float*)d_in[17];
-    const float* normf = (const float*)d_in[18];
-    float* out = (float*)d_out;
-
     char* p = (char*)d_ws;
     auto alloc = [&](size_t bytes) { void* r = p; p += (bytes + 255) & ~255ull; return r; };
     const size_t WQKV = (size_t)HIDN * HH * DD;
     const size_t WMLP = (size_t)HIDN * FFN;
-    u16* WqT = (u16*)alloc(LNUM * WQKV * 2);
-    u16* WkT = (u16*)alloc(LNUM * WQKV * 2);
-    u16* WvT = (u16*)alloc(LNUM * WQKV * 2);
-    u16* WoT = (u16*)alloc(LNUM * WQKV * 2);
-    u16* WgT = (u16*)alloc(LNUM * WMLP * 2);
-    u16* WuT = (u16*)alloc(LNUM * WMLP * 2);
-    u16* WdT = (u16*)alloc(LNUM * WMLP * 2);
-    const int TOK = BB * SS;
-    const size_t EMB_N = (size_t)TOK * HIDN;
-    float* h  = (float*)alloc(EMB_N * 4);
-    u16* qr   = (u16*)alloc((size_t)BB * HH * SS * DD * 2);
-    u16* kr   = (u16*)alloc((size_t)BB * HH * SS * DD * 2);
-    u16* vr   = (u16*)alloc((size_t)BB * HH * SS * DD * 2);
-    u16* oa   = (u16*)alloc(EMB_N * 2);
-    u16* fb   = (u16*)alloc((size_t)TOK * FFN * 2);
-    float* po  = (float*)alloc((size_t)96 * NCH * SS * DD * 4);
-    float* pml = (float*)alloc((size_t)96 * NCH * 32 * 4);
-    float2* tab = (float2*)alloc(16 * 64 * sizeof(float2));
-
-    rope_tab_k<<<16, 64, 0, stream>>>(tab);
-    wtrans_all_k<<<dim3(1728, LNUM), 256, 0, stream>>>(Wq, Wk, Wv, Wo, Wg, Wu, Wd,
-                                                       WqT, WkT, WvT, WoT, WgT, WuT, WdT);
-    hipMemcpyAsync(h, emb, EMB_N * sizeof(float), hipMemcpyDeviceToDevice, stream);
-
-    const size_t KVOFF = (size_t)BB * HH * KVC * DD;
-    for (int l = 0; l < LNUM; ++l) {
-        qkv_k<<<dim3(3 * HH, BB), 256, 0, stream>>>(h, ln1 + l * HIDN,
-            WqT + l * WQKV, WkT + l * WQKV, WvT + l * WQKV,
-            bq + l * HH * DD, bk + l * HH * DD, bv + l * HH * DD, tab, qr, kr, vr);
-        attn_part_k<<<dim3(BB * HH, NCH), 256, 0, stream>>>(qr, kr, vr,
-            k_cache + (size_t)l * KVOFF, v_cache + (size_t)l * KVOFF, po, pml);
-        attn_comb_k<<<BB * HH, 256, 0, stream>>>(po, pml, oa);
-        wo_res_k<<<dim3(12, BB), 256, 0, stream>>>(oa, WoT + l * WQKV, h);
-        ln2gu_k<<<dim3(32, BB), 256, 0, stream>>>(h, ln2 + l * HIDN,
-            WgT + l * WMLP, WuT + l * WMLP, fb);
-        down_res_k<<<dim3(12, BB, 2), 256, 0, stream>>>(fb, WdT + l * WMLP, h);
-    }
-    rmsnorm_f_k<<<TOK, 64, 0, stream>>>(h, normf, out);
+    const size_t EMB_N = (size_t)BB * SS * HIDN;
+
+    MegaArgs ma;
+    ma.emb = (const float*)d_in[0];
+    ma.kc  = (const float*)d_in[4];
+    ma.vc  = (const float*)d_in[5];
+    ma.Wq  = (const float*)d_in[6];
+    ma.bq  = (const float*)d_in[7];
+    ma.Wk  = (const float*)d_in[8];
+    ma.bk  = (const float*)d_in[9];
+    ma.Wv  = (const float*)d_in[10];
+    ma.bv  = (const float*)d_in[11];
+    ma.Wo  = (const float*)d_in[12];
+    ma.Wg  = (const float*)d_in[13];
+    ma.Wu  = (const float*)d_in[14];
+    ma.Wd  = (const float*)d_in[15];
+    ma.ln1 = (const float*)d_in[16];
+    ma.ln2 = (const float*)d_in[17];
+    ma.normf = (const float*)d_in[18];
+    ma.WqT = (u16*)alloc(LNUM * WQKV * 2);
+    ma.WkT = (u16*)alloc(LNUM * WQKV * 2);
+    ma.WvT = (u16*)alloc(LNUM * WQKV * 2);
+    ma.WoT = (u16*)alloc(LNUM * WQKV * 2);
+    ma.WgT = (u16*)alloc(LNUM * WMLP * 2);
+    ma.WuT = (u16*)alloc(LNUM * WMLP * 2);
+    ma.WdT = (u16*)alloc(LNUM * WMLP * 2);
+    ma.h   = (float*)alloc(EMB_N * 4);
+    ma.qr  = (u16*)alloc((size_t)BB * HH * SS * DD * 2);
+    ma.kr  = (u16*)alloc((size_t)BB * HH * SS * DD * 2);
+    ma.vr  = (u16*)alloc((size_t)BB * HH * SS * DD * 2);
+    ma.oa  = (u16*)alloc(EMB_N * 2);
+    ma.fb  = (u16*)alloc((size_t)BB * SS * FFN * 2);
+    ma.po  = (float*)alloc((size_t)96 * NCH * SS * DD * 4);
+    ma.pml = (float*)alloc((size_t)96 * NCH * 32 * 4);
+    ma.tab = (float2*)alloc(16 * 64 * sizeof(float2));
+    ma.out = (float*)d_out;
+
+    int maxb = 0;
+    hipOccupancyMaxActiveBlocksPerMultiprocessor(&maxb, mega_k, 256, 0);
+    if (maxb < 1) maxb = 1;
+    int grid = maxb * 256;
+    if (grid > 1024) grid = 1024;
+
+    void* kargs[] = { (void*)&ma };
+    hipLaunchCooperativeKernel((void*)mega_k, dim3(grid), dim3(256), kargs, 0, stream);
 }
```

After: 1.457 ms. 232% more time.
